# Optimization experiments

Hardware: AMD Instinct MI355X
Metric: run time of the kernel (lower is better)

## Reference

```python
import jax, jax.numpy as jnp
import numpy as np

B, TRG, SRC, ENC, TRGD = 16, 512, 1024, 1024, 1024


def setup_inputs() -> dict:
    key = jax.random.key(0)
    k1, k2, k3, k4, k5 = jax.random.split(key, 5)
    hidden = jax.random.normal(k1, (B, TRG, TRGD), dtype=jnp.float32)
    encoder_outputs = jax.random.normal(k2, (B, SRC, ENC), dtype=jnp.float32)
    encoder_value = jax.random.normal(k3, (B, SRC, TRGD), dtype=jnp.float32)
    # float {0,1} padding mask over source positions; keep first token valid
    encoder_mask = (jax.random.uniform(k4, (B, SRC)) > 0.15).astype(jnp.float32)
    encoder_mask = encoder_mask.at[:, :1].set(1.0)
    # nn.Linear(enc_dim, trg_dim, bias=False).weight -> (trg_dim, enc_dim)
    W = jax.random.normal(k5, (TRGD, ENC), dtype=jnp.float32) * (1.0 / np.sqrt(ENC))
    return {"hidden": hidden, "encoder_outputs": encoder_outputs,
            "encoder_value": encoder_value, "encoder_mask": encoder_mask, "W": W}


def reference(hidden, encoder_outputs, encoder_value, encoder_mask, W):
    # score(): method == 'general'
    proj = jnp.einsum('bse,te->bst', encoder_outputs, W)          # (B, S, trg_dim)
    proj = proj * encoder_mask[:, :, None]                        # mask-multiply projected keys
    energies = jnp.einsum('btd,bsd->bts', hidden, proj)           # (B, T, S)
    # forward(): second mask-multiply on raw energies
    attn_energies = energies * encoder_mask[:, None, :]
    # masked_softmax(x, m, -1): x*m -> stable exp -> *m -> normalize (+eps)
    x = attn_energies * encoder_mask[:, None, :]
    e = jnp.exp(x - jnp.max(x, axis=-1, keepdims=True))
    e = e * encoder_mask[:, None, :]
    attn_weights = e / (jnp.sum(e, axis=-1, keepdims=True) + 1e-6)
    context = jnp.einsum('bts,bsd->btd', attn_weights, encoder_value)  # (B, T, trg_dim)
    return context, attn_weights, attn_energies
```

## Files before the change

### kernel.cpp

```cpp
#include <hip/hip_runtime.h>
#include <hip/hip_bf16.h>
#include <math.h>

#define B_  16
#define T_  512
#define S_  1024
#define E_  1024
#define D_  1024

using short8  = __attribute__((ext_vector_type(8))) short;
using ushort4v = __attribute__((ext_vector_type(4))) unsigned short;
using float4v = __attribute__((ext_vector_type(4))) float;

__device__ __forceinline__ unsigned short f2bf(float f) {
    unsigned u = __builtin_bit_cast(unsigned, f);
    u += 0x7fff + ((u >> 16) & 1);
    return (unsigned short)(u >> 16);
}

__global__ __launch_bounds__(256)
void transpose_cast(const float* __restrict__ src, unsigned short* __restrict__ dst,
                    int R, int C, long long sSrc, long long sDst)
{
    __shared__ unsigned short tile[64][65];
    const int z = blockIdx.z;
    src += (long long)z * sSrc;
    dst += (long long)z * sDst;
    const int c0 = blockIdx.x * 64;
    const int r0 = blockIdx.y * 64;
    const int t = threadIdx.x;

    #pragma unroll
    for (int it = 0; it < 4; ++it) {
        int r  = (t >> 4) + it * 16;
        int c4 = (t & 15) << 2;
        float4 v = *(const float4*)&src[(long long)(r0 + r) * C + c0 + c4];
        tile[r][c4 + 0] = f2bf(v.x);
        tile[r][c4 + 1] = f2bf(v.y);
        tile[r][c4 + 2] = f2bf(v.z);
        tile[r][c4 + 3] = f2bf(v.w);
    }
    __syncthreads();
    #pragma unroll
    for (int it = 0; it < 2; ++it) {
        int c  = (t >> 3) + it * 32;
        int r8 = (t & 7) << 3;
        short8 sv;
        #pragma unroll
        for (int j = 0; j < 8; ++j) sv[j] = (short)tile[r8 + j][c];
        *(short8*)&dst[(long long)(c0 + c) * R + r0 + r8] = sv;
    }
}

template<bool A_F32, bool B_F32, bool OUT_BF16, bool CMASK>
__global__ __launch_bounds__(256)
void mfma_gemm(const void* __restrict__ Ap, const void* __restrict__ Bp,
               const float* __restrict__ mask, void* __restrict__ Cp,
               int N, int K,
               long long sA, long long sB, long long sC, int maskStride)
{
    __shared__ unsigned short Asl[128 * 40];
    __shared__ unsigned short Bsl[128 * 40];

    const int z    = blockIdx.z;
    const int col0 = blockIdx.x * 128;
    const int row0 = blockIdx.y * 128;
    const int t    = threadIdx.x;

    const float*          Af32 = A_F32 ? ((const float*)Ap + z * sA + (long long)row0 * K) : nullptr;
    const unsigned short* Abf  = A_F32 ? nullptr : ((const unsigned short*)Ap + z * sA + (long long)row0 * K);
    const float*          Bf32 = B_F32 ? ((const float*)Bp + z * sB + (long long)col0 * K) : nullptr;
    const unsigned short* Bbf  = B_F32 ? nullptr : ((const unsigned short*)Bp + z * sB + (long long)col0 * K);

    const int lane = t & 63;
    const int wave = t >> 6;
    const int wm = (wave >> 1) * 64;
    const int wn = (wave & 1) * 64;
    const int fr = lane & 15;
    const int fg = lane >> 4;

    float4v acc[4][4];
    #pragma unroll
    for (int i = 0; i < 4; ++i)
        #pragma unroll
        for (int j = 0; j < 4; ++j)
            acc[i][j] = (float4v)0.0f;

    for (int k0 = 0; k0 < K; k0 += 32) {
        if (A_F32) {
            #pragma unroll
            for (int it = 0; it < 4; ++it) {
                int r  = (t >> 3) + it * 32;
                int k4 = (t & 7) << 2;
                float4 v = *(const float4*)&Af32[(long long)r * K + k0 + k4];
                ushort4v u; u[0] = f2bf(v.x); u[1] = f2bf(v.y); u[2] = f2bf(v.z); u[3] = f2bf(v.w);
                *(ushort4v*)&Asl[r * 40 + k4] = u;
            }
        } else {
            #pragma unroll
            for (int it = 0; it < 2; ++it) {
                int r  = (t >> 2) + it * 64;
                int k8 = (t & 3) << 3;
                short8 v = *(const short8*)&Abf[(long long)r * K + k0 + k8];
                *(short8*)&Asl[r * 40 + k8] = v;
            }
        }
        if (B_F32) {
            #pragma unroll
            for (int it = 0; it < 4; ++it) {
                int r  = (t >> 3) + it * 32;
                int k4 = (t & 7) << 2;
                float4 v = *(const float4*)&Bf32[(long long)r * K + k0 + k4];
                ushort4v u; u[0] = f2bf(v.x); u[1] = f2bf(v.y); u[2] = f2bf(v.z); u[3] = f2bf(v.w);
                *(ushort4v*)&Bsl[r * 40 + k4] = u;
            }
        } else {
            #pragma unroll
            for (int it = 0; it < 2; ++it) {
                int r  = (t >> 2) + it * 64;
                int k8 = (t & 3) << 3;
                short8 v = *(const short8*)&Bbf[(long long)r * K + k0 + k8];
                *(short8*)&Bsl[r * 40 + k8] = v;
            }
        }
        __syncthreads();

        short8 af[4], bf[4];
        #pragma unroll
        for (int mi = 0; mi < 4; ++mi)
            af[mi] = *(const short8*)&Asl[(wm + mi * 16 + fr) * 40 + fg * 8];
        #pragma unroll
        for (int ni = 0; ni < 4; ++ni)
            bf[ni] = *(const short8*)&Bsl[(wn + ni * 16 + fr) * 40 + fg * 8];
        #pragma unroll
        for (int mi = 0; mi < 4; ++mi)
            #pragma unroll
            for (int ni = 0; ni < 4; ++ni)
                acc[mi][ni] = __builtin_amdgcn_mfma_f32_16x16x32_bf16(af[mi], bf[ni], acc[mi][ni], 0, 0, 0);
        __syncthreads();
    }

    float mv[4];
    #pragma unroll
    for (int ni = 0; ni < 4; ++ni) {
        int ocol = col0 + wn + ni * 16 + fr;
        mv[ni] = CMASK ? mask[(long long)z * maskStride + ocol] : 1.0f;
    }
    #pragma unroll
    for (int mi = 0; mi < 4; ++mi) {
        #pragma unroll
        for (int ni = 0; ni < 4; ++ni) {
            int ocol = col0 + wn + ni * 16 + fr;
            #pragma unroll
            for (int r = 0; r < 4; ++r) {
                int orow = row0 + wm + mi * 16 + fg * 4 + r;
                float v = acc[mi][ni][r] * mv[ni];
                if (OUT_BF16)
                    ((unsigned short*)Cp)[z * sC + (long long)orow * N + ocol] = f2bf(v);
                else
                    ((float*)Cp)[z * sC + (long long)orow * N + ocol] = v;
            }
        }
    }
}

__global__ __launch_bounds__(256)
void softmax_mask(const float* __restrict__ x, const float* __restrict__ mask,
                  float* __restrict__ w)
{
    const int row = blockIdx.x;
    const int b   = row >> 9;
    const float* xr = x    + (long long)row * S_;
    const float* mr = mask + (long long)b * S_;
    float*       wr = w    + (long long)row * S_;
    const int tid = threadIdx.x;

    float4 xv = ((const float4*)xr)[tid];
    float4 mv = ((const float4*)mr)[tid];

    float lmax = fmaxf(fmaxf(xv.x, xv.y), fmaxf(xv.z, xv.w));
    #pragma unroll
    for (int off = 32; off; off >>= 1)
        lmax = fmaxf(lmax, __shfl_xor(lmax, off, 64));

    __shared__ float red[4];
    const int wave = tid >> 6, lane = tid & 63;
    if (lane == 0) red[wave] = lmax;
    __syncthreads();
    const float rmax = fmaxf(fmaxf(red[0], red[1]), fmaxf(red[2], red[3]));

    float e0 = expf(xv.x - rmax) * mv.x;
    float e1 = expf(xv.y - rmax) * mv.y;
    float e2 = expf(xv.z - rmax) * mv.z;
    float e3 = expf(xv.w - rmax) * mv.w;

    float lsum = (e0 + e1) + (e2 + e3);
    #pragma unroll
    for (int off = 32; off; off >>= 1)
        lsum += __shfl_xor(lsum, off, 64);

    __syncthreads();
    if (lane == 0) red[wave] = lsum;
    __syncthreads();
    const float rsum = (red[0] + red[1]) + (red[2] + red[3]);
    const float inv = 1.0f / (rsum + 1e-6f);

    float4 o;
    o.x = e0 * inv; o.y = e1 * inv; o.z = e2 * inv; o.w = e3 * inv;
    ((float4*)wr)[tid] = o;
}

constexpr int FBM = 64, FBN = 64, FBK = 16;
template<bool BT, bool CMASK>
__global__ __launch_bounds__(256)
void gemm_f32(const float* __restrict__ A, const float* __restrict__ Bm,
              const float* __restrict__ mask, float* __restrict__ C,
              int N_dim, int K_dim,
              long long sA, long long sB, long long sC, int maskStride)
{
    const int bz = blockIdx.z;
    A  += (long long)bz * sA;
    Bm += (long long)bz * sB;
    C  += (long long)bz * sC;
    __shared__ float As[FBK][FBM];
    __shared__ float Bs[FBK][FBN];
    const int tid  = threadIdx.x;
    const int row0 = blockIdx.y * FBM;
    const int col0 = blockIdx.x * FBN;
    const int lrow = tid >> 2;
    const int lk   = (tid & 3) << 2;
    const int bk = tid >> 4;
    const int bn = (tid & 15) << 2;
    const int tx = tid & 15;
    const int ty = tid >> 4;
    float acc[4][4] = {};
    const float* Aptr = A + (long long)(row0 + lrow) * K_dim + lk;
    const float* Bptr = BT ? (Bm + (long long)(col0 + lrow) * K_dim + lk)
                           : (Bm + (long long)bk * N_dim + col0 + bn);
    for (int k0 = 0; k0 < K_dim; k0 += FBK) {
        float4 av = *(const float4*)(Aptr + k0);
        As[lk + 0][lrow] = av.x; As[lk + 1][lrow] = av.y;
        As[lk + 2][lrow] = av.z; As[lk + 3][lrow] = av.w;
        if (BT) {
            float4 bv = *(const float4*)(Bptr + k0);
            Bs[lk + 0][lrow] = bv.x; Bs[lk + 1][lrow] = bv.y;
            Bs[lk + 2][lrow] = bv.z; Bs[lk + 3][lrow] = bv.w;
        } else {
            float4 bv = *(const float4*)(Bptr + (long long)k0 * N_dim);
            *(float4*)&Bs[bk][bn] = bv;
        }
        __syncthreads();
        #pragma unroll
        for (int k = 0; k < FBK; ++k) {
            float4 a4 = *(const float4*)&As[k][ty << 2];
            float4 b4 = *(const float4*)&Bs[k][tx << 2];
            float ar[4] = {a4.x, a4.y, a4.z, a4.w};
            float br[4] = {b4.x, b4.y, b4.z, b4.w};
            #pragma unroll
            for (int i = 0; i < 4; ++i)
                #pragma unroll
                for (int j = 0; j < 4; ++j)
                    acc[i][j] = fmaf(ar[i], br[j], acc[i][j]);
        }
        __syncthreads();
    }
    float mvv[4] = {1.f, 1.f, 1.f, 1.f};
    if (CMASK) {
        #pragma unroll
        for (int j = 0; j < 4; ++j)
            mvv[j] = mask[(long long)bz * maskStride + col0 + (tx << 2) + j];
    }
    #pragma unroll
    for (int i = 0; i < 4; ++i) {
        const int r = row0 + (ty << 2) + i;
        float4 o;
        o.x = acc[i][0] * mvv[0]; o.y = acc[i][1] * mvv[1];
        o.z = acc[i][2] * mvv[2]; o.w = acc[i][3] * mvv[3];
        *(float4*)&C[(long long)r * N_dim + col0 + (tx << 2)] = o;
    }
}

extern "C" void kernel_launch(void* const* d_in, const int* in_sizes, int n_in,
                              void* d_out, int out_size, void* d_ws, size_t ws_size,
                              hipStream_t stream)
{
    const float* hidden = (const float*)d_in[0];
    const float* eo     = (const float*)d_in[1];
    const float* ev     = (const float*)d_in[2];
    const float* mask   = (const float*)d_in[3];
    const float* W      = (const float*)d_in[4];

    float* out = (float*)d_out;
    const long long CTX = (long long)B_ * T_ * D_;
    float* ctx = out;
    float* aw  = out + CTX;
    float* ae  = out + 2 * CTX;

    const size_t WT_BYTES  = (size_t)E_ * D_ * 2;
    const size_t EVT_BYTES = (size_t)B_ * D_ * S_ * 2;
    const size_t G_BYTES   = (size_t)B_ * T_ * E_ * 2;
    const size_t NEED = WT_BYTES + EVT_BYTES + G_BYTES;

    dim3 blk(256);

    if (ws_size >= NEED) {
        unsigned short* WT  = (unsigned short*)d_ws;
        unsigned short* EVT = (unsigned short*)((char*)d_ws + WT_BYTES);
        unsigned short* G   = (unsigned short*)((char*)d_ws + WT_BYTES + EVT_BYTES);

        transpose_cast<<<dim3(E_ / 64, D_ / 64, 1), blk, 0, stream>>>(
            W, WT, D_, E_, 0, 0);
        transpose_cast<<<dim3(D_ / 64, S_ / 64, B_), blk, 0, stream>>>(
            ev, EVT, S_, D_, (long long)S_ * D_, (long long)D_ * S_);

        mfma_gemm<true, false, true, false><<<dim3(E_ / 128, (B_ * T_) / 128, 1), blk, 0, stream>>>(
            hidden, WT, nullptr, G, E_, D_, 0, 0, 0, 0);

        mfma_gemm<false, true, false, true><<<dim3(S_ / 128, T_ / 128, B_), blk, 0, stream>>>(
            G, eo, mask, ae, S_, E_,
            (long long)T_ * E_, (long long)S_ * E_, (long long)T_ * S_, S_);

        softmax_mask<<<dim3(B_ * T_), blk, 0, stream>>>(ae, mask, aw);

        mfma_gemm<true, false, false, false><<<dim3(D_ / 128, T_ / 128, B_), blk, 0, stream>>>(
            aw, EVT, nullptr, ctx, D_, S_,
            (long long)T_ * S_, (long long)D_ * S_, (long long)T_ * D_, 0);
    } else {
        float* G = aw;
        gemm_f32<false, false><<<dim3(E_ / FBN, (B_ * T_) / FBM, 1), blk, 0, stream>>>(
            hidden, W, nullptr, G, E_, D_, 0, 0, 0, 0);
        gemm_f32<true, true><<<dim3(S_ / FBN, T_ / FBM, B_), blk, 0, stream>>>(
            G, eo, mask, ae, S_, E_,
            (long long)T_ * E_, (long long)S_ * E_, (long long)T_ * S_, S_);
        softmax_mask<<<dim3(B_ * T_), blk, 0, stream>>>(ae, mask, aw);
        gemm_f32<false, false><<<dim3(D_ / FBN, T_ / FBM, B_), blk, 0, stream>>>(
            aw, ev, nullptr, ctx, D_, S_,
            (long long)T_ * S_, (long long)S_ * D_, (long long)T_ * D_, 0);
    }
}
```

Baseline: 359.4 us.

## Pre-cast GEMM operands to bf16 and stage tiles via direct global-to-LDS loads

Adds a new fast path, used when the workspace holds at least 64 MB. Hidden and encoder_outputs are pre-cast to bf16 in separate kernels, and softmax additionally writes a bf16 copy of the attention weights. All three GEMMs then read bf16 operands and load tiles with global_load_lds straight into unpadded LDS. This removes the in-loop fp32 loads and conversions and the register round trip through LDS. In exchange it adds extra passes over the inputs, reuses workspace regions with careful ordering, and the unpadded LDS layout may cause bank conflicts.

```diff
diff --git a/kernel.cpp b/kernel.cpp
--- a/kernel.cpp
+++ b/kernel.cpp
@@ -1,5 +1,4 @@
 #include <hip/hip_runtime.h>
-#include <hip/hip_bf16.h>
 #include <math.h>
 
 #define B_  16
@@ -8,14 +7,34 @@
 #define E_  1024
 #define D_  1024
 
-using short8  = __attribute__((ext_vector_type(8))) short;
+using short8   = __attribute__((ext_vector_type(8))) short;
 using ushort4v = __attribute__((ext_vector_type(4))) unsigned short;
-using float4v = __attribute__((ext_vector_type(4))) float;
+using float4v  = __attribute__((ext_vector_type(4))) float;
 
 __device__ __forceinline__ unsigned short f2bf(float f) {
     unsigned u = __builtin_bit_cast(unsigned, f);
     u += 0x7fff + ((u >> 16) & 1);
     return (unsigned short)(u >> 16);
+}
+
+__device__ __forceinline__ void gl_lds16(const void* g, void* l) {
+    __builtin_amdgcn_global_load_lds(
+        (const __attribute__((address_space(1))) void*)g,
+        (__attribute__((address_space(3))) void*)l, 16, 0, 0);
+}
+
+__global__ __launch_bounds__(256)
+void cast_bf16(const float* __restrict__ src, unsigned short* __restrict__ dst, int n8)
+{
+    int i = blockIdx.x * 256 + threadIdx.x;
+    if (i < n8) {
+        float4 a = ((const float4*)src)[2 * i];
+        float4 b = ((const float4*)src)[2 * i + 1];
+        short8 o;
+        o[0] = f2bf(a.x); o[1] = f2bf(a.y); o[2] = f2bf(a.z); o[3] = f2bf(a.w);
+        o[4] = f2bf(b.x); o[5] = f2bf(b.y); o[6] = f2bf(b.z); o[7] = f2bf(b.w);
+        ((short8*)dst)[i] = o;
+    }
 }
 
 __global__ __launch_bounds__(256)
@@ -52,28 +71,31 @@
     }
 }
 
-template<bool A_F32, bool B_F32, bool OUT_BF16, bool CMASK>
-__global__ __launch_bounds__(256)
-void mfma_gemm(const void* __restrict__ Ap, const void* __restrict__ Bp,
-               const float* __restrict__ mask, void* __restrict__ Cp,
-               int N, int K,
-               long long sA, long long sB, long long sC, int maskStride)
-{
-    __shared__ unsigned short Asl[128 * 40];
-    __shared__ unsigned short Bsl[128 * 40];
+template<bool OUT_BF16, bool CMASK>
+__global__ __launch_bounds__(256)
+void mfma_gemm_bf(const unsigned short* __restrict__ Ap,
+                  const unsigned short* __restrict__ Bp,
+                  const float* __restrict__ mask, void* __restrict__ Cp,
+                  int N, int K,
+                  long long sA, long long sB, long long sC, int maskStride)
+{
+    __shared__ unsigned short Asl[128 * 32];
+    __shared__ unsigned short Bsl[128 * 32];
 
     const int z    = blockIdx.z;
     const int col0 = blockIdx.x * 128;
     const int row0 = blockIdx.y * 128;
     const int t    = threadIdx.x;
-
-    const float*          Af32 = A_F32 ? ((const float*)Ap + z * sA + (long long)row0 * K) : nullptr;
-    const unsigned short* Abf  = A_F32 ? nullptr : ((const unsigned short*)Ap + z * sA + (long long)row0 * K);
-    const float*          Bf32 = B_F32 ? ((const float*)Bp + z * sB + (long long)col0 * K) : nullptr;
-    const unsigned short* Bbf  = B_F32 ? nullptr : ((const unsigned short*)Bp + z * sB + (long long)col0 * K);
-
     const int lane = t & 63;
     const int wave = t >> 6;
+
+    const unsigned short* A  = Ap + z * sA + (long long)row0 * K;
+    const unsigned short* Bm = Bp + z * sB + (long long)col0 * K;
+
+    const int rs  = t >> 2;
+    const int kcs = (t & 3) << 3;
+    const unsigned ldsW = wave * 1024;
+
     const int wm = (wave >> 1) * 64;
     const int wn = (wave & 1) * 64;
     const int fr = lane & 15;
@@ -87,51 +109,21 @@
             acc[i][j] = (float4v)0.0f;
 
     for (int k0 = 0; k0 < K; k0 += 32) {
-        if (A_F32) {
-            #pragma unroll
-            for (int it = 0; it < 4; ++it) {
-                int r  = (t >> 3) + it * 32;
-                int k4 = (t & 7) << 2;
-                float4 v = *(const float4*)&Af32[(long long)r * K + k0 + k4];
-                ushort4v u; u[0] = f2bf(v.x); u[1] = f2bf(v.y); u[2] = f2bf(v.z); u[3] = f2bf(v.w);
-                *(ushort4v*)&Asl[r * 40 + k4] = u;
-            }
-        } else {
-            #pragma unroll
-            for (int it = 0; it < 2; ++it) {
-                int r  = (t >> 2) + it * 64;
-                int k8 = (t & 3) << 3;
-                short8 v = *(const short8*)&Abf[(long long)r * K + k0 + k8];
-                *(short8*)&Asl[r * 40 + k8] = v;
-            }
-        }
-        if (B_F32) {
-            #pragma unroll
-            for (int it = 0; it < 4; ++it) {
-                int r  = (t >> 3) + it * 32;
-                int k4 = (t & 7) << 2;
-                float4 v = *(const float4*)&Bf32[(long long)r * K + k0 + k4];
-                ushort4v u; u[0] = f2bf(v.x); u[1] = f2bf(v.y); u[2] = f2bf(v.z); u[3] = f2bf(v.w);
-                *(ushort4v*)&Bsl[r * 40 + k4] = u;
-            }
-        } else {
-            #pragma unroll
-            for (int it = 0; it < 2; ++it) {
-                int r  = (t >> 2) + it * 64;
-                int k8 = (t & 3) << 3;
-                short8 v = *(const short8*)&Bbf[(long long)r * K + k0 + k8];
-                *(short8*)&Bsl[r * 40 + k8] = v;
-            }
+        #pragma unroll
+        for (int it = 0; it < 2; ++it) {
+            const int r = rs + it * 64;
+            gl_lds16(A  + (long long)r * K + k0 + kcs, (char*)Asl + ldsW + it * 4096);
+            gl_lds16(Bm + (long long)r * K + k0 + kcs, (char*)Bsl + ldsW + it * 4096);
         }
         __syncthreads();
 
         short8 af[4], bf[4];
         #pragma unroll
         for (int mi = 0; mi < 4; ++mi)
-            af[mi] = *(const short8*)&Asl[(wm + mi * 16 + fr) * 40 + fg * 8];
+            af[mi] = *(const short8*)&Asl[(wm + mi * 16 + fr) * 32 + fg * 8];
         #pragma unroll
         for (int ni = 0; ni < 4; ++ni)
-            bf[ni] = *(const short8*)&Bsl[(wn + ni * 16 + fr) * 40 + fg * 8];
+            bf[ni] = *(const short8*)&Bsl[(wn + ni * 16 + fr) * 32 + fg * 8];
         #pragma unroll
         for (int mi = 0; mi < 4; ++mi)
             #pragma unroll
@@ -164,9 +156,121 @@
     }
 }
 
+template<bool A_F32, bool B_F32, bool OUT_BF16, bool CMASK>
+__global__ __launch_bounds__(256)
+void mfma_gemm(const void* __restrict__ Ap, const void* __restrict__ Bp,
+               const float* __restrict__ mask, void* __restrict__ Cp,
+               int N, int K,
+               long long sA, long long sB, long long sC, int maskStride)
+{
+    __shared__ unsigned short Asl[128 * 40];
+    __shared__ unsigned short Bsl[128 * 40];
+
+    const int z    = blockIdx.z;
+    const int col0 = blockIdx.x * 128;
+    const int row0 = blockIdx.y * 128;
+    const int t    = threadIdx.x;
+
+    const float*          Af32 = A_F32 ? ((const float*)Ap + z * sA + (long long)row0 * K) : nullptr;
+    const unsigned short* Abf  = A_F32 ? nullptr : ((const unsigned short*)Ap + z * sA + (long long)row0 * K);
+    const float*          Bf32 = B_F32 ? ((const float*)Bp + z * sB + (long long)col0 * K) : nullptr;
+    const unsigned short* Bbf  = B_F32 ? nullptr : ((const unsigned short*)Bp + z * sB + (long long)col0 * K);
+
+    const int lane = t & 63;
+    const int wave = t >> 6;
+    const int wm = (wave >> 1) * 64;
+    const int wn = (wave & 1) * 64;
+    const int fr = lane & 15;
+    const int fg = lane >> 4;
+
+    float4v acc[4][4];
+    #pragma unroll
+    for (int i = 0; i < 4; ++i)
+        #pragma unroll
+        for (int j = 0; j < 4; ++j)
+            acc[i][j] = (float4v)0.0f;
+
+    for (int k0 = 0; k0 < K; k0 += 32) {
+        if (A_F32) {
+            #pragma unroll
+            for (int it = 0; it < 4; ++it) {
+                int r  = (t >> 3) + it * 32;
+                int k4 = (t & 7) << 2;
+                float4 v = *(const float4*)&Af32[(long long)r * K + k0 + k4];
+                ushort4v u; u[0] = f2bf(v.x); u[1] = f2bf(v.y); u[2] = f2bf(v.z); u[3] = f2bf(v.w);
+                *(ushort4v*)&Asl[r * 40 + k4] = u;
+            }
+        } else {
+            #pragma unroll
+            for (int it = 0; it < 2; ++it) {
+                int r  = (t >> 2) + it * 64;
+                int k8 = (t & 3) << 3;
+                short8 v = *(const short8*)&Abf[(long long)r * K + k0 + k8];
+                *(short8*)&Asl[r * 40 + k8] = v;
+            }
+        }
+        if (B_F32) {
+            #pragma unroll
+            for (int it = 0; it < 4; ++it) {
+                int r  = (t >> 3) + it * 32;
+                int k4 = (t & 7) << 2;
+                float4 v = *(const float4*)&Bf32[(long long)r * K + k0 + k4];
+                ushort4v u; u[0] = f2bf(v.x); u[1] = f2bf(v.y); u[2] = f2bf(v.z); u[3] = f2bf(v.w);
+                *(ushort4v*)&Bsl[r * 40 + k4] = u;
+            }
+        } else {
+            #pragma unroll
+            for (int it = 0; it < 2; ++it) {
+                int r  = (t >> 2) + it * 64;
+                int k8 = (t & 3) << 3;
+                short8 v = *(const short8*)&Bbf[(long long)r * K + k0 + k8];
+                *(short8*)&Bsl[r * 40 + k8] = v;
+            }
+        }
+        __syncthreads();
+
+        short8 af[4], bf[4];
+        #pragma unroll
+        for (int mi = 0; mi < 4; ++mi)
+            af[mi] = *(const short8*)&Asl[(wm + mi * 16 + fr) * 40 + fg * 8];
+        #pragma unroll
+        for (int ni = 0; ni < 4; ++ni)
+            bf[ni] = *(const short8*)&Bsl[(wn + ni * 16 + fr) * 40 + fg * 8];
+        #pragma unroll
+        for (int mi = 0; mi < 4; ++mi)
+            #pragma unroll
+            for (int ni = 0; ni < 4; ++ni)
+                acc[mi][ni] = __builtin_amdgcn_mfma_f32_16x16x32_bf16(af[mi], bf[ni], acc[mi][ni], 0, 0, 0);
+        __syncthreads();
+    }
+
+    float mv[4];
+    #pragma unroll
+    for (int ni = 0; ni < 4; ++ni) {
+        int ocol = col0 + wn + ni * 16 + fr;
+        mv[ni] = CMASK ? mask[(long long)z * maskStride + ocol] : 1.0f;
+    }
+    #pragma unroll
+    for (int mi = 0; mi < 4; ++mi) {
+        #pragma unroll
+        for (int ni = 0; ni < 4; ++ni) {
+            int ocol = col0 + wn + ni * 16 + fr;
+            #pragma unroll
+            for (int r = 0; r < 4; ++r) {
+                int orow = row0 + wm + mi * 16 + fg * 4 + r;
+                float v = acc[mi][ni][r] * mv[ni];
+                if (OUT_BF16)
+                    ((unsigned short*)Cp)[z * sC + (long long)orow * N + ocol] = f2bf(v);
+                else
+                    ((float*)Cp)[z * sC + (long long)orow * N + ocol] = v;
+            }
+        }
+    }
+}
+
 __global__ __launch_bounds__(256)
 void softmax_mask(const float* __restrict__ x, const float* __restrict__ mask,
-                  float* __restrict__ w)
+                  float* __restrict__ w, unsigned short* __restrict__ wbf)
 {
     const int row = blockIdx.x;
     const int b   = row >> 9;
@@ -208,6 +312,11 @@
     float4 o;
     o.x = e0 * inv; o.y = e1 * inv; o.z = e2 * inv; o.w = e3 * inv;
     ((float4*)wr)[tid] = o;
+    if (wbf) {
+        ushort4v u;
+        u[0] = f2bf(o.x); u[1] = f2bf(o.y); u[2] = f2bf(o.z); u[3] = f2bf(o.w);
+        ((ushort4v*)(wbf + (long long)row * S_))[tid] = u;
+    }
 }
 
 constexpr int FBM = 64, FBN = 64, FBK = 16;
@@ -296,32 +405,59 @@
     float* aw  = out + CTX;
     float* ae  = out + 2 * CTX;
 
-    const size_t WT_BYTES  = (size_t)E_ * D_ * 2;
-    const size_t EVT_BYTES = (size_t)B_ * D_ * S_ * 2;
-    const size_t G_BYTES   = (size_t)B_ * T_ * E_ * 2;
-    const size_t NEED = WT_BYTES + EVT_BYTES + G_BYTES;
-
     dim3 blk(256);
 
-    if (ws_size >= NEED) {
+    const size_t MB = 1024ull * 1024ull;
+    const size_t NEED_FAST = 64 * MB;
+    const size_t NEED_MID  = 50 * MB;
+
+    if (ws_size >= NEED_FAST) {
+        char* ws = (char*)d_ws;
+        unsigned short* Hbf  = (unsigned short*)(ws);
+        unsigned short* WT   = (unsigned short*)(ws + 16 * MB);
+        unsigned short* EObf = (unsigned short*)(ws);
+        unsigned short* EVT  = (unsigned short*)(ws + 16 * MB);
+        unsigned short* G    = (unsigned short*)(ws + 48 * MB);
+        unsigned short* AWbf = (unsigned short*)(ws + 48 * MB);
+
+        cast_bf16<<<dim3((B_ * T_ * D_ / 8 + 255) / 256), blk, 0, stream>>>(
+            hidden, Hbf, B_ * T_ * D_ / 8);
+        transpose_cast<<<dim3(E_ / 64, D_ / 64, 1), blk, 0, stream>>>(
+            W, WT, D_, E_, 0, 0);
+
+        mfma_gemm_bf<true, false><<<dim3(E_ / 128, (B_ * T_) / 128, 1), blk, 0, stream>>>(
+            Hbf, WT, nullptr, G, E_, D_, 0, 0, 0, 0);
+
+        cast_bf16<<<dim3((B_ * S_ * E_ / 8 + 255) / 256), blk, 0, stream>>>(
+            eo, EObf, B_ * S_ * E_ / 8);
+
+        mfma_gemm_bf<false, true><<<dim3(S_ / 128, T_ / 128, B_), blk, 0, stream>>>(
+            G, EObf, mask, ae, S_, E_,
+            (long long)T_ * E_, (long long)S_ * E_, (long long)T_ * S_, S_);
+
+        transpose_cast<<<dim3(D_ / 64, S_ / 64, B_), blk, 0, stream>>>(
+            ev, EVT, S_, D_, (long long)S_ * D_, (long long)D_ * S_);
+
+        softmax_mask<<<dim3(B_ * T_), blk, 0, stream>>>(ae, mask, aw, AWbf);
+
+        mfma_gemm_bf<false, false><<<dim3(D_ / 128, T_ / 128, B_), blk, 0, stream>>>(
+            AWbf, EVT, nullptr, ctx, D_, S_,
+            (long long)T_ * S_, (long long)D_ * S_, (long long)T_ * D_, 0);
+    } else if (ws_size >= NEED_MID) {
         unsigned short* WT  = (unsigned short*)d_ws;
-        unsigned short* EVT = (unsigned short*)((char*)d_ws + WT_BYTES);
-        unsigned short* G   = (unsigned short*)((char*)d_ws + WT_BYTES + EVT_BYTES);
+        unsigned short* EVT = (unsigned short*)((char*)d_ws + 2 * MB);
+        unsigned short* G   = (unsigned short*)((char*)d_ws + 34 * MB);
 
         transpose_cast<<<dim3(E_ / 64, D_ / 64, 1), blk, 0, stream>>>(
             W, WT, D_, E_, 0, 0);
         transpose_cast<<<dim3(D_ / 64, S_ / 64, B_), blk, 0, stream>>>(
             ev, EVT, S_, D_, (long long)S_ * D_, (long long)D_ * S_);
-
         mfma_gemm<true, false, true, false><<<dim3(E_ / 128, (B_ * T_) / 128, 1), blk, 0, stream>>>(
             hidden, WT, nullptr, G, E_, D_, 0, 0, 0, 0);
-
         mfma_gemm<false, true, false, true><<<dim3(S_ / 128, T_ / 128, B_), blk, 0, stream>>>(
             G, eo, mask, ae, S_, E_,
             (long long)T_ * E_, (long long)S_ * E_, (long long)T_ * S_, S_);
-
-        softmax_mask<<<dim3(B_ * T_), blk, 0, stream>>>(ae, mask, aw);
-
+        softmax_mask<<<dim3(B_ * T_), blk, 0, stream>>>(ae, mask, aw, nullptr);
         mfma_gemm<true, false, false, false><<<dim3(D_ / 128, T_ / 128, B_), blk, 0, stream>>>(
             aw, EVT, nullptr, ctx, D_, S_,
             (long long)T_ * S_, (long long)D_ * S_, (long long)T_ * D_, 0);
@@ -332,7 +468,7 @@
         gemm_f32<true, true><<<dim3(S_ / FBN, T_ / FBM, B_), blk, 0, stream>>>(
             G, eo, mask, ae, S_, E_,
             (long long)T_ * E_, (long long)S_ * E_, (long long)T_ * S_, S_);
-        softmax_mask<<<dim3(B_ * T_), blk, 0, stream>>>(ae, mask, aw);
+        softmax_mask<<<dim3(B_ * T_), blk, 0, stream>>>(ae, mask, aw, nullptr);
         gemm_f32<false, false><<<dim3(D_ / FBN, T_ / FBM, B_), blk, 0, stream>>>(
             aw, ev, nullptr, ctx, D_, S_,
             (long long)T_ * S_, (long long)S_ * D_, (long long)T_ * D_, 0);
```

New measurement: 340.0 us. 1.06x faster.

## Pre-cast GEMM operands to bf16 and stream tiles via global-to-LDS loads

Applied to the files above, without the earlier changes.

Hidden and encoder_outputs are cast to bf16 in separate elementwise passes, and softmax writes an extra bf16 copy of the attention weights. All three GEMMs can then use one bf16-only MFMA kernel. That kernel loads tiles with direct global_load_lds, unpadded, processes 64 K elements per barrier pair, and requests two blocks per CU. This removes the fp32 loads and in-loop conversion from the GEMM inner loops and halves operand traffic. The cost is extra cast passes, aliased workspace buffers, a 64MB workspace requirement, and possible LDS bank conflicts from the unpadded layout.

```diff
diff --git a/kernel.cpp b/kernel.cpp
--- a/kernel.cpp
+++ b/kernel.cpp
@@ -1,5 +1,4 @@
 #include <hip/hip_runtime.h>
-#include <hip/hip_bf16.h>
 #include <math.h>
 
 #define B_  16
@@ -8,14 +7,34 @@
 #define E_  1024
 #define D_  1024
 
-using short8  = __attribute__((ext_vector_type(8))) short;
+using short8   = __attribute__((ext_vector_type(8))) short;
 using ushort4v = __attribute__((ext_vector_type(4))) unsigned short;
-using float4v = __attribute__((ext_vector_type(4))) float;
+using float4v  = __attribute__((ext_vector_type(4))) float;
 
 __device__ __forceinline__ unsigned short f2bf(float f) {
     unsigned u = __builtin_bit_cast(unsigned, f);
     u += 0x7fff + ((u >> 16) & 1);
     return (unsigned short)(u >> 16);
+}
+
+__device__ __forceinline__ void gl_lds16(const void* g, void* l) {
+    __builtin_amdgcn_global_load_lds(
+        (const __attribute__((address_space(1))) void*)g,
+        (__attribute__((address_space(3))) void*)l, 16, 0, 0);
+}
+
+__global__ __launch_bounds__(256)
+void cast_bf16(const float* __restrict__ src, unsigned short* __restrict__ dst, int n8)
+{
+    int i = blockIdx.x * 256 + threadIdx.x;
+    if (i < n8) {
+        float4 a = ((const float4*)src)[2 * i];
+        float4 b = ((const float4*)src)[2 * i + 1];
+        short8 o;
+        o[0] = f2bf(a.x); o[1] = f2bf(a.y); o[2] = f2bf(a.z); o[3] = f2bf(a.w);
+        o[4] = f2bf(b.x); o[5] = f2bf(b.y); o[6] = f2bf(b.z); o[7] = f2bf(b.w);
+        ((short8*)dst)[i] = o;
+    }
 }
 
 __global__ __launch_bounds__(256)
@@ -52,28 +71,31 @@
     }
 }
 
-template<bool A_F32, bool B_F32, bool OUT_BF16, bool CMASK>
-__global__ __launch_bounds__(256)
-void mfma_gemm(const void* __restrict__ Ap, const void* __restrict__ Bp,
-               const float* __restrict__ mask, void* __restrict__ Cp,
-               int N, int K,
-               long long sA, long long sB, long long sC, int maskStride)
-{
-    __shared__ unsigned short Asl[128 * 40];
-    __shared__ unsigned short Bsl[128 * 40];
+template<bool OUT_BF16, bool CMASK>
+__global__ __launch_bounds__(256, 2)
+void mfma_gemm_bf(const unsigned short* __restrict__ Ap,
+                  const unsigned short* __restrict__ Bp,
+                  const float* __restrict__ mask, void* __restrict__ Cp,
+                  int N, int K,
+                  long long sA, long long sB, long long sC, int maskStride)
+{
+    __shared__ unsigned short Asl[2 * 128 * 32];
+    __shared__ unsigned short Bsl[2 * 128 * 32];
 
     const int z    = blockIdx.z;
     const int col0 = blockIdx.x * 128;
     const int row0 = blockIdx.y * 128;
     const int t    = threadIdx.x;
-
-    const float*          Af32 = A_F32 ? ((const float*)Ap + z * sA + (long long)row0 * K) : nullptr;
-    const unsigned short* Abf  = A_F32 ? nullptr : ((const unsigned short*)Ap + z * sA + (long long)row0 * K);
-    const float*          Bf32 = B_F32 ? ((const float*)Bp + z * sB + (long long)col0 * K) : nullptr;
-    const unsigned short* Bbf  = B_F32 ? nullptr : ((const unsigned short*)Bp + z * sB + (long long)col0 * K);
-
     const int lane = t & 63;
     const int wave = t >> 6;
+
+    const unsigned short* A  = Ap + z * sA + (long long)row0 * K;
+    const unsigned short* Bm = Bp + z * sB + (long long)col0 * K;
+
+    const int rs  = t >> 2;
+    const int kcs = (t & 3) << 3;
+    const unsigned ldsW = wave * 1024;
+
     const int wm = (wave >> 1) * 64;
     const int wn = (wave & 1) * 64;
     const int fr = lane & 15;
@@ -86,57 +108,37 @@
         for (int j = 0; j < 4; ++j)
             acc[i][j] = (float4v)0.0f;
 
-    for (int k0 = 0; k0 < K; k0 += 32) {
-        if (A_F32) {
-            #pragma unroll
-            for (int it = 0; it < 4; ++it) {
-                int r  = (t >> 3) + it * 32;
-                int k4 = (t & 7) << 2;
-                float4 v = *(const float4*)&Af32[(long long)r * K + k0 + k4];
-                ushort4v u; u[0] = f2bf(v.x); u[1] = f2bf(v.y); u[2] = f2bf(v.z); u[3] = f2bf(v.w);
-                *(ushort4v*)&Asl[r * 40 + k4] = u;
+    for (int k0 = 0; k0 < K; k0 += 64) {
+        #pragma unroll
+        for (int j = 0; j < 2; ++j) {
+            #pragma unroll
+            for (int it = 0; it < 2; ++it) {
+                const int r = rs + it * 64;
+                const long long goff = (long long)r * K + k0 + j * 32 + kcs;
+                const unsigned loff = j * 8192 + it * 4096 + ldsW;
+                gl_lds16(A  + goff, (char*)Asl + loff);
+                gl_lds16(Bm + goff, (char*)Bsl + loff);
             }
-        } else {
-            #pragma unroll
-            for (int it = 0; it < 2; ++it) {
-                int r  = (t >> 2) + it * 64;
-                int k8 = (t & 3) << 3;
-                short8 v = *(const short8*)&Abf[(long long)r * K + k0 + k8];
-                *(short8*)&Asl[r * 40 + k8] = v;
-            }
-        }
-        if (B_F32) {
-            #pragma unroll
-            for (int it = 0; it < 4; ++it) {
-                int r  = (t >> 3) + it * 32;
-                int k4 = (t & 7) << 2;
-                float4 v = *(const float4*)&Bf32[(long long)r * K + k0 + k4];
-                ushort4v u; u[0] = f2bf(v.x); u[1] = f2bf(v.y); u[2] = f2bf(v.z); u[3] = f2bf(v.w);
-                *(ushort4v*)&Bsl[r * 40 + k4] = u;
-            }
-        } else {
-            #pragma unroll
-            for (int it = 0; it < 2; ++it) {
-                int r  = (t >> 2) + it * 64;
-                int k8 = (t & 3) << 3;
-                short8 v = *(const short8*)&Bbf[(long long)r * K + k0 + k8];
-                *(short8*)&Bsl[r * 40 + k8] = v;
-            }
         }
         __syncthreads();
 
-        short8 af[4], bf[4];
-        #pragma unroll
-        for (int mi = 0; mi < 4; ++mi)
-            af[mi] = *(const short8*)&Asl[(wm + mi * 16 + fr) * 40 + fg * 8];
-        #pragma unroll
-        for (int ni = 0; ni < 4; ++ni)
-            bf[ni] = *(const short8*)&Bsl[(wn + ni * 16 + fr) * 40 + fg * 8];
-        #pragma unroll
-        for (int mi = 0; mi < 4; ++mi)
+        short8 af[2][4], bf[2][4];
+        #pragma unroll
+        for (int j = 0; j < 2; ++j) {
+            #pragma unroll
+            for (int mi = 0; mi < 4; ++mi)
+                af[j][mi] = *(const short8*)&Asl[j * 4096 + (wm + mi * 16 + fr) * 32 + fg * 8];
             #pragma unroll
             for (int ni = 0; ni < 4; ++ni)
-                acc[mi][ni] = __builtin_amdgcn_mfma_f32_16x16x32_bf16(af[mi], bf[ni], acc[mi][ni], 0, 0, 0);
+                bf[j][ni] = *(const short8*)&Bsl[j * 4096 + (wn + ni * 16 + fr) * 32 + fg * 8];
+        }
+        #pragma unroll
+        for (int j = 0; j < 2; ++j)
+            #pragma unroll
+            for (int mi = 0; mi < 4; ++mi)
+                #pragma unroll
+                for (int ni = 0; ni < 4; ++ni)
+                    acc[mi][ni] = __builtin_amdgcn_mfma_f32_16x16x32_bf16(af[j][mi], bf[j][ni], acc[mi][ni], 0, 0, 0);
         __syncthreads();
     }
 
@@ -166,7 +168,7 @@
 
 __global__ __launch_bounds__(256)
 void softmax_mask(const float* __restrict__ x, const float* __restrict__ mask,
-                  float* __restrict__ w)
+                  float* __restrict__ w, unsigned short* __restrict__ wbf)
 {
     const int row = blockIdx.x;
     const int b   = row >> 9;
@@ -208,6 +210,11 @@
     float4 o;
     o.x = e0 * inv; o.y = e1 * inv; o.z = e2 * inv; o.w = e3 * inv;
     ((float4*)wr)[tid] = o;
+    if (wbf) {
+        ushort4v u;
+        u[0] = f2bf(o.x); u[1] = f2bf(o.y); u[2] = f2bf(o.z); u[3] = f2bf(o.w);
+        ((ushort4v*)(wbf + (long long)row * S_))[tid] = u;
+    }
 }
 
 constexpr int FBM = 64, FBN = 64, FBK = 16;
@@ -296,34 +303,41 @@
     float* aw  = out + CTX;
     float* ae  = out + 2 * CTX;
 
-    const size_t WT_BYTES  = (size_t)E_ * D_ * 2;
-    const size_t EVT_BYTES = (size_t)B_ * D_ * S_ * 2;
-    const size_t G_BYTES   = (size_t)B_ * T_ * E_ * 2;
-    const size_t NEED = WT_BYTES + EVT_BYTES + G_BYTES;
-
     dim3 blk(256);
-
-    if (ws_size >= NEED) {
-        unsigned short* WT  = (unsigned short*)d_ws;
-        unsigned short* EVT = (unsigned short*)((char*)d_ws + WT_BYTES);
-        unsigned short* G   = (unsigned short*)((char*)d_ws + WT_BYTES + EVT_BYTES);
-
+    const size_t MB = 1024ull * 1024ull;
+    const size_t NEED_FAST = 64 * MB;
+
+    if (ws_size >= NEED_FAST) {
+        char* ws = (char*)d_ws;
+        unsigned short* Hbf  = (unsigned short*)(ws);
+        unsigned short* WT   = (unsigned short*)(ws + 16 * MB);
+        unsigned short* EObf = (unsigned short*)(ws);
+        unsigned short* EVT  = (unsigned short*)(ws + 16 * MB);
+        unsigned short* G    = (unsigned short*)(ws + 48 * MB);
+        unsigned short* AWbf = (unsigned short*)(ws + 48 * MB);
+
+        cast_bf16<<<dim3((B_ * T_ * D_ / 8 + 255) / 256), blk, 0, stream>>>(
+            hidden, Hbf, B_ * T_ * D_ / 8);
         transpose_cast<<<dim3(E_ / 64, D_ / 64, 1), blk, 0, stream>>>(
             W, WT, D_, E_, 0, 0);
+
+        mfma_gemm_bf<true, false><<<dim3(E_ / 128, (B_ * T_) / 128, 1), blk, 0, stream>>>(
+            Hbf, WT, nullptr, G, E_, D_, 0, 0, 0, 0);
+
+        cast_bf16<<<dim3((B_ * S_ * E_ / 8 + 255) / 256), blk, 0, stream>>>(
+            eo, EObf, B_ * S_ * E_ / 8);
+
+        mfma_gemm_bf<false, true><<<dim3(S_ / 128, T_ / 128, B_), blk, 0, stream>>>(
+            G, EObf, mask, ae, S_, E_,
+            (long long)T_ * E_, (long long)S_ * E_, (long long)T_ * S_, S_);
+
         transpose_cast<<<dim3(D_ / 64, S_ / 64, B_), blk, 0, stream>>>(
             ev, EVT, S_, D_, (long long)S_ * D_, (long long)D_ * S_);
 
-        mfma_gemm<true, false, true, false><<<dim3(E_ / 128, (B_ * T_) / 128, 1), blk, 0, stream>>>(
-            hidden, WT, nullptr, G, E_, D_, 0, 0, 0, 0);
-
-        mfma_gemm<false, true, false, true><<<dim3(S_ / 128, T_ / 128, B_), blk, 0, stream>>>(
-            G, eo, mask, ae, S_, E_,
-            (long long)T_ * E_, (long long)S_ * E_, (long long)T_ * S_, S_);
-
-        softmax_mask<<<dim3(B_ * T_), blk, 0, stream>>>(ae, mask, aw);
-
-        mfma_gemm<true, false, false, false><<<dim3(D_ / 128, T_ / 128, B_), blk, 0, stream>>>(
-            aw, EVT, nullptr, ctx, D_, S_,
+        softmax_mask<<<dim3(B_ * T_), blk, 0, stream>>>(ae, mask, aw, AWbf);
+
+        mfma_gemm_bf<false, false><<<dim3(D_ / 128, T_ / 128, B_), blk, 0, stream>>>(
+            AWbf, EVT, nullptr, ctx, D_, S_,
             (long long)T_ * S_, (long long)D_ * S_, (long long)T_ * D_, 0);
     } else {
         float* G = aw;
@@ -332,7 +346,7 @@
         gemm_f32<true, true><<<dim3(S_ / FBN, T_ / FBM, B_), blk, 0, stream>>>(
             G, eo, mask, ae, S_, E_,
             (long long)T_ * E_, (long long)S_ * E_, (long long)T_ * S_, S_);
-        softmax_mask<<<dim3(B_ * T_), blk, 0, stream>>>(ae, mask, aw);
+        softmax_mask<<<dim3(B_ * T_), blk, 0, stream>>>(ae, mask, aw, nullptr);
         gemm_f32<false, false><<<dim3(D_ / FBN, T_ / FBM, B_), blk, 0, stream>>>(
             aw, ev, nullptr, ctx, D_, S_,
             (long long)T_ * S_, (long long)S_ * D_, (long long)T_ * D_, 0);
```

Result: faster. 319.0 us (-11.2%).
